# Kernel tuning notes

Hardware: AMD Instinct MI355X
Metric: run time of the kernel (lower is better)

Reference implementation:

```python
import jax, jax.numpy as jnp
import numpy as np

B, T, D, A = 32, 4096, 256, 128

def setup_inputs() -> dict:
    key = jax.random.key(0)
    k1, k2, k3, k4 = jax.random.split(key, 4)
    return {
        "h": jax.random.normal(k1, (B, T, D), dtype=jnp.float32),
        "W_w": jax.random.normal(k2, (A, D), dtype=jnp.float32),
        "b_w": jax.random.normal(k3, (A,), dtype=jnp.float32),
        "u_w": jax.random.normal(k4, (A,), dtype=jnp.float32),
    }

def reference(h, W_w, b_w, u_w):
    # u = tanh(h @ W_w^T + b_w)  -> [B, T, A]
    u = jnp.tanh(jnp.einsum("btd,ad->bta", h, W_w) + b_w)
    # score = u . u_w            -> [B, T]
    score = jnp.einsum("bta,a->bt", u, u_w)
    # softmax over sequence axis (stable form of exp/sum in original)
    alpha = jax.nn.softmax(score, axis=-1)  # [B, T]
    # weighted sum pooling over T -> [B, D]
    s = jnp.einsum("bt,btd->bd", alpha, h)
    return s
```

## Files before the change

### kernel.cpp

```cpp
#include <hip/hip_runtime.h>

#define B_ 32
#define T_ 4096
#define D_ 256
#define A_ 128

typedef __attribute__((ext_vector_type(8))) short bf16x8;
typedef __attribute__((ext_vector_type(4))) float f32x4;
typedef __attribute__((address_space(3))) void lds_void_t;
typedef const __attribute__((address_space(1))) void gbl_void_t;

__device__ __forceinline__ float bf16_bits_to_f32(ushort b) {
    return __uint_as_float(((uint)b) << 16);
}

__device__ __forceinline__ float fast_tanh(float x) {
    float t = __expf(2.0f * x);
    float r = __builtin_amdgcn_rcpf(t + 1.0f);
    return fmaf(-2.0f, r, 1.0f);
}

__device__ __forceinline__ void split8(float4 a, float4 b, bf16x8& hi8, bf16x8& lo8) {
    float xs[8] = {a.x, a.y, a.z, a.w, b.x, b.y, b.z, b.w};
    union { uint w[4]; bf16x8 v; } H, L;
#pragma unroll
    for (int p = 0; p < 4; ++p) {
        float x0 = xs[2 * p], x1 = xs[2 * p + 1];
        uint r0 = __float_as_uint(x0) + 0x8000u;
        uint r1 = __float_as_uint(x1) + 0x8000u;
        H.w[p] = __builtin_amdgcn_perm(r1, r0, 0x07060302u);
        float rem0 = x0 - __uint_as_float(r0 & 0xFFFF0000u);
        float rem1 = x1 - __uint_as_float(r1 & 0xFFFF0000u);
        L.w[p] = __builtin_amdgcn_perm(__float_as_uint(rem1), __float_as_uint(rem0), 0x07060302u);
    }
    hi8 = H.v;
    lo8 = L.v;
}

__global__ __launch_bounds__(512, 2) void score_pool_kernel(
    const float* __restrict__ h, const float* __restrict__ W,
    const float* __restrict__ bw, const float* __restrict__ uw,
    float* __restrict__ part, float2* __restrict__ stats)
{
    __shared__ char smem[163840];
    char* wlds = smem;
    char* ht   = smem + 131072;

    const int tid  = threadIdx.x;
    const int w    = tid >> 6;
    const int lane = tid & 63;
    const int l15  = lane & 15;
    const int l4   = lane >> 4;
    const int blk  = blockIdx.x;
    const size_t blkrow = (size_t)blk * 512;

    float bwv[8], uwv[8];
#pragma unroll
    for (int j = 0; j < 8; ++j) { bwv[j] = bw[j * 16 + l15]; uwv[j] = uw[j * 16 + l15]; }
    __builtin_amdgcn_sched_barrier(0);

    const float* hlane = h + (blkrow + (size_t)w * 16 + l15) * D_ + l4 * 4;

#define HSTAGE(s2, buf)                                                         \
    {                                                                           \
        const float* s0_ = hlane + (size_t)((s2) >> 3) * 128 * D_ + ((s2) & 7) * 32; \
        char* d_ = ht + (buf) * 16384 + w * 2048;                               \
        __builtin_amdgcn_global_load_lds((gbl_void_t*)(s0_),      (lds_void_t*)(d_),        16, 0, 0); \
        __builtin_amdgcn_global_load_lds((gbl_void_t*)(s0_ + 16), (lds_void_t*)(d_ + 1024), 16, 0, 0); \
    }

    HSTAGE(0, 0);
    HSTAGE(1, 1);
    __builtin_amdgcn_sched_barrier(0);

#pragma unroll
    for (int i = 0; i < 8; ++i) {
        const int cc  = i * 512 + tid;
        const int ph  = cc >> 10;
        const int rem = cc & 1023;
        const int r   = rem >> 3;
        const int sp  = rem & 7;
        const int sx  = sp ^ (r & 7);
        const float* src = W + (size_t)r * D_ + ph * 64 + sx * 8;
        float4 a = *reinterpret_cast<const float4*>(src);
        float4 b = *reinterpret_cast<const float4*>(src + 4);
        bf16x8 hi, lo;
        split8(a, b, hi, lo);
        const int base = ph * 32768 + r * 128 + sp * 16;
        *reinterpret_cast<bf16x8*>(wlds + base)         = hi;
        *reinterpret_cast<bf16x8*>(wlds + 16384 + base) = lo;
    }
    asm volatile("s_waitcnt lgkmcnt(0)" ::: "memory");
    __builtin_amdgcn_sched_barrier(0);
    __builtin_amdgcn_s_barrier();
    __builtin_amdgcn_sched_barrier(0);

    const int reg0 = (l4 >> 1) * 1024;
    const int rd0  = w * 2048 + reg0 + (((l4 * 2)     & 3) * 16 + l15) * 16;
    const int rd1  = w * 2048 + reg0 + (((l4 * 2 + 1) & 3) * 16 + l15) * 16;

    f32x4 acc[8];
#pragma unroll
    for (int j = 0; j < 8; ++j)
#pragma unroll
        for (int r = 0; r < 4; ++r) acc[j][r] = 0.f;

    float4 pacc[4];
    float  m_arr[4], s_arr[4];

#pragma unroll
    for (int s = 0; s < 32; ++s) {
        const int g   = s >> 3;
        const int kk  = s & 7;
        const int buf = s & 1;

        if (s == 31) { asm volatile("s_waitcnt vmcnt(0)" ::: "memory"); }
        else         { asm volatile("s_waitcnt vmcnt(2)" ::: "memory"); }
        __builtin_amdgcn_sched_barrier(0);

        float4 x0 = *reinterpret_cast<const float4*>(ht + buf * 16384 + rd0);
        float4 x1 = *reinterpret_cast<const float4*>(ht + buf * 16384 + rd1);
        asm volatile("s_waitcnt lgkmcnt(0)" ::: "memory");
        __builtin_amdgcn_sched_barrier(0);
        if (s + 2 < 32) HSTAGE(s + 2, buf);

        bf16x8 ahi, alo;
        split8(x0, x1, ahi, alo);

        const int chunk = kk >> 1;
        const int slot  = (kk & 1) * 4 + l4;
#pragma unroll
        for (int j = 0; j < 8; ++j) {
            const int row = j * 16 + l15;
            const int off = chunk * 32768 + row * 128 + ((slot ^ (row & 7)) << 4);
            bf16x8 wh = *reinterpret_cast<const bf16x8*>(wlds + off);
            bf16x8 wl = *reinterpret_cast<const bf16x8*>(wlds + 16384 + off);
            acc[j] = __builtin_amdgcn_mfma_f32_16x16x32_bf16(ahi, wh, acc[j], 0, 0, 0);
            acc[j] = __builtin_amdgcn_mfma_f32_16x16x32_bf16(alo, wh, acc[j], 0, 0, 0);
            acc[j] = __builtin_amdgcn_mfma_f32_16x16x32_bf16(ahi, wl, acc[j], 0, 0, 0);
        }

        if (kk == 7) {
            float rsum[4] = {0.f, 0.f, 0.f, 0.f};
#pragma unroll
            for (int j = 0; j < 8; ++j)
#pragma unroll
                for (int r = 0; r < 4; ++r) {
                    rsum[r] = fmaf(fast_tanh(acc[j][r] + bwv[j]), uwv[j], rsum[r]);
                    acc[j][r] = 0.f;
                }
#pragma unroll
            for (int r = 0; r < 4; ++r) {
#pragma unroll
                for (int m = 1; m < 16; m <<= 1)
                    rsum[r] += __shfl_xor(rsum[r], m, 64);
            }
            float sc16[16];
#pragma unroll
            for (int rr = 0; rr < 16; ++rr)
                sc16[rr] = __shfl(rsum[rr & 3], (rr >> 2) << 4, 64);

            float m_w = sc16[0];
#pragma unroll
            for (int rr = 1; rr < 16; ++rr) m_w = fmaxf(m_w, sc16[rr]);
            float e16[16], s_w = 0.f;
#pragma unroll
            for (int rr = 0; rr < 16; ++rr) { e16[rr] = __expf(sc16[rr] - m_w); s_w += e16[rr]; }

            const float* hg = h + (blkrow + (size_t)g * 128 + w * 16) * D_ + lane * 4;
            float4 pg = {0.f, 0.f, 0.f, 0.f};
#pragma unroll
            for (int r = 0; r < 16; ++r) {
                float4 v = *reinterpret_cast<const float4*>(hg + (size_t)r * D_);
                pg.x = fmaf(e16[r], v.x, pg.x);
                pg.y = fmaf(e16[r], v.y, pg.y);
                pg.z = fmaf(e16[r], v.z, pg.z);
                pg.w = fmaf(e16[r], v.w, pg.w);
            }
            pacc[g]  = pg;
            m_arr[g] = m_w;
            s_arr[g] = s_w;

            asm volatile("s_waitcnt vmcnt(0)" ::: "memory");
            __builtin_amdgcn_sched_barrier(0);
        }
    }
#undef HSTAGE

    float2* mst = (float2*)wlds;
    float*  Pl  = (float*)ht;
    __syncthreads();
#pragma unroll
    for (int g = 0; g < 4; ++g) {
        const int cid = g * 8 + w;
        *reinterpret_cast<float4*>(Pl + cid * 256 + lane * 4) = pacc[g];
        if (lane == 0) mst[cid] = make_float2(m_arr[g], s_arr[g]);
    }
    __syncthreads();
    if (tid < 256) {
        float M = -3.0e38f;
#pragma unroll
        for (int c = 0; c < 32; ++c) M = fmaxf(M, mst[c].x);
        float wc[32], S = 0.f;
#pragma unroll
        for (int c = 0; c < 32; ++c) {
            wc[c] = __expf(mst[c].x - M);
            S = fmaf(wc[c], mst[c].y, S);
        }
        float p = 0.f;
#pragma unroll
        for (int c = 0; c < 32; ++c) p = fmaf(wc[c], Pl[c * 256 + tid], p);
        part[(size_t)blk * 256 + tid] = p;
        if (tid == 0) stats[blk] = make_float2(M, S);
    }
}

__global__ __launch_bounds__(256) void combine_kernel(
    const float* __restrict__ part, const float2* __restrict__ stats,
    float* __restrict__ out)
{
    const int b = blockIdx.x;
    const int t = threadIdx.x;

    float m8[8], s8[8];
    float Mg = -3.0e38f;
#pragma unroll
    for (int c = 0; c < 8; ++c) {
        float2 st = stats[b * 8 + c];
        m8[c] = st.x; s8[c] = st.y;
        Mg = fmaxf(Mg, st.x);
    }
    float wc[8], S = 0.f;
#pragma unroll
    for (int c = 0; c < 8; ++c) {
        wc[c] = __expf(m8[c] - Mg);
        S = fmaf(wc[c], s8[c], S);
    }
    const float invS = 1.0f / S;

    float acc = 0.f;
#pragma unroll
    for (int c = 0; c < 8; ++c)
        acc = fmaf(wc[c], part[((size_t)b * 8 + c) * D_ + t], acc);
    out[b * D_ + t] = acc * invS;
}

extern "C" void kernel_launch(void* const* d_in, const int* in_sizes, int n_in,
                              void* d_out, int out_size, void* d_ws, size_t ws_size,
                              hipStream_t stream) {
    const float* h  = (const float*)d_in[0];
    const float* W  = (const float*)d_in[1];
    const float* bw = (const float*)d_in[2];
    const float* uw = (const float*)d_in[3];
    float* out = (float*)d_out;

    float*  part  = (float*)d_ws;
    float2* stats = (float2*)(part + (size_t)256 * D_);

    score_pool_kernel<<<dim3(256), 512, 0, stream>>>(h, W, bw, uw, part, stats);
    combine_kernel<<<dim3(B_), 256, 0, stream>>>(part, stats, out);
}
```

Baseline: 47.68 us.

## Process two 16-row tiles per wave to reuse W fragments across twice the MFMAs

Each wave now handles 32 sequence rows per group (two accumulator sets) instead of 16, so every W hi/lo fragment read from LDS feeds six MFMAs instead of three. The double-buffered h staging is replaced by a single buffer holding twice the data, with a full vmcnt(0) wait before each step, and the number of groups per block drops from four to two. This cuts LDS traffic for W per MFMA but doubles accumulator registers and removes load/compute overlap, which risks exposing global-to-LDS latency and lowering occupancy.

```diff
diff --git a/kernel.cpp b/kernel.cpp
--- a/kernel.cpp
+++ b/kernel.cpp
@@ -59,18 +59,21 @@
     for (int j = 0; j < 8; ++j) { bwv[j] = bw[j * 16 + l15]; uwv[j] = uw[j * 16 + l15]; }
     __builtin_amdgcn_sched_barrier(0);
 
-    const float* hlane = h + (blkrow + (size_t)w * 16 + l15) * D_ + l4 * 4;
-
-#define HSTAGE(s2, buf)                                                         \
+    const float* hlA = h + (blkrow + (size_t)w * 32 + l15) * D_ + l4 * 4;
+
+#define HSTAGE(s2)                                                              \
     {                                                                           \
-        const float* s0_ = hlane + (size_t)((s2) >> 3) * 128 * D_ + ((s2) & 7) * 32; \
-        char* d_ = ht + (buf) * 16384 + w * 2048;                               \
-        __builtin_amdgcn_global_load_lds((gbl_void_t*)(s0_),      (lds_void_t*)(d_),        16, 0, 0); \
-        __builtin_amdgcn_global_load_lds((gbl_void_t*)(s0_ + 16), (lds_void_t*)(d_ + 1024), 16, 0, 0); \
-    }
-
-    HSTAGE(0, 0);
-    HSTAGE(1, 1);
+        const int g_ = (s2) >> 3, kk_ = (s2) & 7;                               \
+        const float* sA = hlA + (size_t)g_ * 256 * D_ + kk_ * 32;               \
+        const float* sB = sA + 16 * D_;                                         \
+        char* d_ = ht + w * 4096;                                               \
+        __builtin_amdgcn_global_load_lds((gbl_void_t*)(sA),      (lds_void_t*)(d_),        16, 0, 0); \
+        __builtin_amdgcn_global_load_lds((gbl_void_t*)(sA + 16), (lds_void_t*)(d_ + 1024), 16, 0, 0); \
+        __builtin_amdgcn_global_load_lds((gbl_void_t*)(sB),      (lds_void_t*)(d_ + 2048), 16, 0, 0); \
+        __builtin_amdgcn_global_load_lds((gbl_void_t*)(sB + 16), (lds_void_t*)(d_ + 3072), 16, 0, 0); \
+    }
+
+    HSTAGE(0);
     __builtin_amdgcn_sched_barrier(0);
 
 #pragma unroll
@@ -96,93 +99,102 @@
     __builtin_amdgcn_sched_barrier(0);
 
     const int reg0 = (l4 >> 1) * 1024;
-    const int rd0  = w * 2048 + reg0 + (((l4 * 2)     & 3) * 16 + l15) * 16;
-    const int rd1  = w * 2048 + reg0 + (((l4 * 2 + 1) & 3) * 16 + l15) * 16;
-
-    f32x4 acc[8];
+    const int rdA0 = w * 4096 + reg0 + (((l4 * 2)     & 3) * 16 + l15) * 16;
+    const int rdA1 = w * 4096 + reg0 + (((l4 * 2 + 1) & 3) * 16 + l15) * 16;
+
+    f32x4 acc0[8], acc1[8];
 #pragma unroll
     for (int j = 0; j < 8; ++j)
 #pragma unroll
-        for (int r = 0; r < 4; ++r) acc[j][r] = 0.f;
-
-    float4 pacc[4];
-    float  m_arr[4], s_arr[4];
-
-#pragma unroll
-    for (int s = 0; s < 32; ++s) {
-        const int g   = s >> 3;
-        const int kk  = s & 7;
-        const int buf = s & 1;
-
-        if (s == 31) { asm volatile("s_waitcnt vmcnt(0)" ::: "memory"); }
-        else         { asm volatile("s_waitcnt vmcnt(2)" ::: "memory"); }
+        for (int r = 0; r < 4; ++r) { acc0[j][r] = 0.f; acc1[j][r] = 0.f; }
+
+    float4 pacc[2];
+    float  m_arr[2], s_arr[2];
+
+#pragma unroll
+    for (int s = 0; s < 16; ++s) {
+        const int g  = s >> 3;
+        const int kk = s & 7;
+
+        asm volatile("s_waitcnt vmcnt(0)" ::: "memory");
         __builtin_amdgcn_sched_barrier(0);
 
-        float4 x0 = *reinterpret_cast<const float4*>(ht + buf * 16384 + rd0);
-        float4 x1 = *reinterpret_cast<const float4*>(ht + buf * 16384 + rd1);
+        float4 x0 = *reinterpret_cast<const float4*>(ht + rdA0);
+        float4 x1 = *reinterpret_cast<const float4*>(ht + rdA1);
+        float4 x2 = *reinterpret_cast<const float4*>(ht + rdA0 + 2048);
+        float4 x3 = *reinterpret_cast<const float4*>(ht + rdA1 + 2048);
         asm volatile("s_waitcnt lgkmcnt(0)" ::: "memory");
         __builtin_amdgcn_sched_barrier(0);
-        if (s + 2 < 32) HSTAGE(s + 2, buf);
-
-        bf16x8 ahi, alo;
-        split8(x0, x1, ahi, alo);
+        if (s < 15) HSTAGE(s + 1);
+
+        bf16x8 ahi0, alo0, ahi1, alo1;
+        split8(x0, x1, ahi0, alo0);
+        split8(x2, x3, ahi1, alo1);
 
         const int chunk = kk >> 1;
-        const int slot  = (kk & 1) * 4 + l4;
+        const int slotb = (kk & 1) * 4 + l4;
 #pragma unroll
         for (int j = 0; j < 8; ++j) {
             const int row = j * 16 + l15;
-            const int off = chunk * 32768 + row * 128 + ((slot ^ (row & 7)) << 4);
+            const int off = chunk * 32768 + row * 128 + ((slotb ^ (row & 7)) << 4);
             bf16x8 wh = *reinterpret_cast<const bf16x8*>(wlds + off);
             bf16x8 wl = *reinterpret_cast<const bf16x8*>(wlds + 16384 + off);
-            acc[j] = __builtin_amdgcn_mfma_f32_16x16x32_bf16(ahi, wh, acc[j], 0, 0, 0);
-            acc[j] = __builtin_amdgcn_mfma_f32_16x16x32_bf16(alo, wh, acc[j], 0, 0, 0);
-            acc[j] = __builtin_amdgcn_mfma_f32_16x16x32_bf16(ahi, wl, acc[j], 0, 0, 0);
+            acc0[j] = __builtin_amdgcn_mfma_f32_16x16x32_bf16(ahi0, wh, acc0[j], 0, 0, 0);
+            acc0[j] = __builtin_amdgcn_mfma_f32_16x16x32_bf16(alo0, wh, acc0[j], 0, 0, 0);
+            acc0[j] = __builtin_amdgcn_mfma_f32_16x16x32_bf16(ahi0, wl, acc0[j], 0, 0, 0);
+            acc1[j] = __builtin_amdgcn_mfma_f32_16x16x32_bf16(ahi1, wh, acc1[j], 0, 0, 0);
+            acc1[j] = __builtin_amdgcn_mfma_f32_16x16x32_bf16(alo1, wh, acc1[j], 0, 0, 0);
+            acc1[j] = __builtin_amdgcn_mfma_f32_16x16x32_bf16(ahi1, wl, acc1[j], 0, 0, 0);
         }
 
         if (kk == 7) {
-            float rsum[4] = {0.f, 0.f, 0.f, 0.f};
+            float rsum0[4] = {0.f, 0.f, 0.f, 0.f};
+            float rsum1[4] = {0.f, 0.f, 0.f, 0.f};
 #pragma unroll
             for (int j = 0; j < 8; ++j)
 #pragma unroll
                 for (int r = 0; r < 4; ++r) {
-                    rsum[r] = fmaf(fast_tanh(acc[j][r] + bwv[j]), uwv[j], rsum[r]);
-                    acc[j][r] = 0.f;
+                    rsum0[r] = fmaf(fast_tanh(acc0[j][r] + bwv[j]), uwv[j], rsum0[r]);
+                    rsum1[r] = fmaf(fast_tanh(acc1[j][r] + bwv[j]), uwv[j], rsum1[r]);
+                    acc0[j][r] = 0.f;
+                    acc1[j][r] = 0.f;
                 }
 #pragma unroll
             for (int r = 0; r < 4; ++r) {
 #pragma unroll
-                for (int m = 1; m < 16; m <<= 1)
-                    rsum[r] += __shfl_xor(rsum[r], m, 64);
+                for (int m = 1; m < 16; m <<= 1) {
+                    rsum0[r] += __shfl_xor(rsum0[r], m, 64);
+                    rsum1[r] += __shfl_xor(rsum1[r], m, 64);
+                }
             }
-            float sc16[16];
-#pragma unroll
-            for (int rr = 0; rr < 16; ++rr)
-                sc16[rr] = __shfl(rsum[rr & 3], (rr >> 2) << 4, 64);
-
-            float m_w = sc16[0];
-#pragma unroll
-            for (int rr = 1; rr < 16; ++rr) m_w = fmaxf(m_w, sc16[rr]);
-            float e16[16], s_w = 0.f;
-#pragma unroll
-            for (int rr = 0; rr < 16; ++rr) { e16[rr] = __expf(sc16[rr] - m_w); s_w += e16[rr]; }
-
-            const float* hg = h + (blkrow + (size_t)g * 128 + w * 16) * D_ + lane * 4;
+            float sc32[32];
+#pragma unroll
+            for (int q = 0; q < 4; ++q)
+#pragma unroll
+                for (int r = 0; r < 4; ++r) {
+                    sc32[q * 4 + r]      = __shfl(rsum0[r], q << 4, 64);
+                    sc32[16 + q * 4 + r] = __shfl(rsum1[r], q << 4, 64);
+                }
+            float m_w = sc32[0];
+#pragma unroll
+            for (int rr = 1; rr < 32; ++rr) m_w = fmaxf(m_w, sc32[rr]);
+
+            const float* hg = h + (blkrow + (size_t)g * 256 + w * 32) * D_ + lane * 4;
             float4 pg = {0.f, 0.f, 0.f, 0.f};
-#pragma unroll
-            for (int r = 0; r < 16; ++r) {
+            float s_w = 0.f;
+#pragma unroll
+            for (int r = 0; r < 32; ++r) {
+                const float e = __expf(sc32[r] - m_w);
+                s_w += e;
                 float4 v = *reinterpret_cast<const float4*>(hg + (size_t)r * D_);
-                pg.x = fmaf(e16[r], v.x, pg.x);
-                pg.y = fmaf(e16[r], v.y, pg.y);
-                pg.z = fmaf(e16[r], v.z, pg.z);
-                pg.w = fmaf(e16[r], v.w, pg.w);
+                pg.x = fmaf(e, v.x, pg.x);
+                pg.y = fmaf(e, v.y, pg.y);
+                pg.z = fmaf(e, v.z, pg.z);
+                pg.w = fmaf(e, v.w, pg.w);
             }
             pacc[g]  = pg;
             m_arr[g] = m_w;
             s_arr[g] = s_w;
-
-            asm volatile("s_waitcnt vmcnt(0)" ::: "memory");
-            __builtin_amdgcn_sched_barrier(0);
         }
     }
 #undef HSTAGE
@@ -191,7 +203,7 @@
     float*  Pl  = (float*)ht;
     __syncthreads();
 #pragma unroll
-    for (int g = 0; g < 4; ++g) {
+    for (int g = 0; g < 2; ++g) {
         const int cid = g * 8 + w;
         *reinterpret_cast<float4*>(Pl + cid * 256 + lane * 4) = pacc[g];
         if (lane == 0) mst[cid] = make_float2(m_arr[g], s_arr[g]);
@@ -200,16 +212,16 @@
     if (tid < 256) {
         float M = -3.0e38f;
 #pragma unroll
-        for (int c = 0; c < 32; ++c) M = fmaxf(M, mst[c].x);
-        float wc[32], S = 0.f;
-#pragma unroll
-        for (int c = 0; c < 32; ++c) {
+        for (int c = 0; c < 16; ++c) M = fmaxf(M, mst[c].x);
+        float wc[16], S = 0.f;
+#pragma unroll
+        for (int c = 0; c < 16; ++c) {
             wc[c] = __expf(mst[c].x - M);
             S = fmaf(wc[c], mst[c].y, S);
         }
         float p = 0.f;
 #pragma unroll
-        for (int c = 0; c < 32; ++c) p = fmaf(wc[c], Pl[c * 256 + tid], p);
+        for (int c = 0; c < 16; ++c) p = fmaf(wc[c], Pl[c * 256 + tid], p);
         part[(size_t)blk * 256 + tid] = p;
         if (tid == 0) stats[blk] = make_float2(M, S);
     }
```

Result: slower. 51.44 us (+7.9%).
